# Optimization experiments

Hardware: AMD Instinct MI355X
Metric: run time of the kernel (lower is better)

## Reference

```python
import jax, jax.numpy as jnp
import numpy as np

B, S, HID = 2, 2048, 1024
H, D = 16, 64  # num query heads, head_dim; single shared KV head
SCALE = D ** -0.5


def setup_inputs() -> dict:
    key = jax.random.key(0)
    k1, k2, k3, k4, k5 = jax.random.split(key, 5)
    return {
        "hidden_states": jax.random.normal(k1, (B, S, HID), dtype=jnp.float32),
        "Wq": jax.random.normal(k2, (HID, HID), dtype=jnp.float32) * 0.02,
        "Wk": jax.random.normal(k3, (HID, D), dtype=jnp.float32) * 0.02,
        "Wv": jax.random.normal(k4, (HID, D), dtype=jnp.float32) * 0.02,
        "Wo": jax.random.normal(k5, (HID, HID), dtype=jnp.float32) * 0.02,
    }


def reference(hidden_states, Wq, Wk, Wv, Wo):
    b, s, _ = hidden_states.shape
    # projections: Q has H heads; K/V have a single shared head of dim D
    q = (hidden_states @ Wq).reshape(b, s, H, D)  # [B,S,H,D]
    k = hidden_states @ Wk                        # [B,S,D]
    v = hidden_states @ Wv                        # [B,S,D]
    # scores: broadcast single KV head across all query heads
    scores = jnp.einsum("bqhd,bkd->bhqk", q, k) * SCALE  # [B,H,S,S]
    attn = jax.nn.softmax(scores, axis=-1)
    out = jnp.einsum("bhqk,bkd->bqhd", attn, v).reshape(b, s, HID)
    return out @ Wo
```

## Files before the change

kernel.cpp:

```cpp
#include <hip/hip_runtime.h>
#include <math.h>

#define BATCH 2
#define SEQ   2048
#define HID   1024
#define NH    16
#define HD    64
#define MTOT  (BATCH * SEQ)

#define PST 72
#define WTS 69

#define EXP_C1 0.1803368801111255f
#define EXP_C2 (-17.312340490667562f)

typedef __attribute__((ext_vector_type(8))) short short8;
typedef __attribute__((ext_vector_type(4))) float floatx4;
typedef __attribute__((ext_vector_type(16))) float floatx16;
typedef __attribute__((ext_vector_type(4))) unsigned int uint4v;

#define MFMA32(a, b, c) __builtin_amdgcn_mfma_f32_32x32x16_bf16(a, b, c, 0, 0, 0)

static __device__ __forceinline__ floatx16 zero16() {
    floatx16 z;
    #pragma unroll
    for (int i = 0; i < 16; ++i) z[i] = 0.f;
    return z;
}

__device__ __forceinline__ unsigned short f2bf(float x) {
    unsigned u = __float_as_uint(x);
    u += 0x7FFF + ((u >> 16) & 1);
    return (unsigned short)(u >> 16);
}
__device__ __forceinline__ float bf2f(unsigned short h) {
    return __uint_as_float((unsigned)h << 16);
}
__device__ __forceinline__ unsigned pack2bf(float lo, float hi) {
    return (unsigned)f2bf(lo) | ((unsigned)f2bf(hi) << 16);
}
__device__ __forceinline__ void split16(const float* f, unsigned short* hh, unsigned short* ll) {
    #pragma unroll
    for (int e = 0; e < 16; ++e) {
        unsigned short h = f2bf(f[e]);
        hh[e] = h;
        ll[e] = f2bf(f[e] - bf2f(h));
    }
}

__global__ __launch_bounds__(256)
void presplit_kernel(const float* __restrict__ Wq, const float* __restrict__ Wk,
                     const float* __restrict__ Wv, const float* __restrict__ Wo,
                     const float* __restrict__ X,
                     unsigned short* __restrict__ WqTh, unsigned short* __restrict__ WqTl,
                     unsigned short* __restrict__ WkTh, unsigned short* __restrict__ WkTl,
                     unsigned short* __restrict__ WvTh, unsigned short* __restrict__ WvTl,
                     unsigned short* __restrict__ WoTh, unsigned short* __restrict__ WoTl,
                     unsigned short* __restrict__ Xh)
{
    __shared__ __align__(16) float Wtmp[64][WTS];
    const int tid = threadIdx.x;
    int bx = blockIdx.x;

    if (bx >= 544) {
        size_t i0 = (size_t)(bx - 544) * 4096 + tid * 16;
        float f[16];
        *(float4*)&f[0]  = *(const float4*)(X + i0 + 0);
        *(float4*)&f[4]  = *(const float4*)(X + i0 + 4);
        *(float4*)&f[8]  = *(const float4*)(X + i0 + 8);
        *(float4*)&f[12] = *(const float4*)(X + i0 + 12);
        unsigned short hh[16];
        #pragma unroll
        for (int e = 0; e < 16; ++e) hh[e] = f2bf(f[e]);
        *(uint4*)(Xh + i0)     = *(uint4*)&hh[0];
        *(uint4*)(Xh + i0 + 8) = *(uint4*)&hh[8];
        return;
    }

    const float* W; unsigned short *Th, *Tl; int ldw, kt, nt;
    if (bx < 256)      { W = Wq; Th = WqTh; Tl = WqTl; ldw = HID; kt = bx >> 4; nt = bx & 15; }
    else if (bx < 272) { W = Wk; Th = WkTh; Tl = WkTl; ldw = HD;  kt = bx - 256; nt = 0; }
    else if (bx < 288) { W = Wv; Th = WvTh; Tl = WvTl; ldw = HD;  kt = bx - 272; nt = 0; }
    else               { W = Wo; Th = WoTh; Tl = WoTl; ldw = HID; bx -= 288; kt = bx >> 4; nt = bx & 15; }
    const int k0 = kt * 64, n0 = nt * 64;

    {
        const int wk = tid >> 2, wn = (tid & 3) * 16;
        const float* wp = W + (size_t)(k0 + wk) * ldw + n0 + wn;
        float f[16];
        *(float4*)&f[0]  = *(const float4*)(wp + 0);
        *(float4*)&f[4]  = *(const float4*)(wp + 4);
        *(float4*)&f[8]  = *(const float4*)(wp + 8);
        *(float4*)&f[12] = *(const float4*)(wp + 12);
        #pragma unroll
        for (int e = 0; e < 16; ++e) Wtmp[wk][wn + e] = f[e];
    }
    __syncthreads();
    {
        const int rn = tid >> 2, rk = (tid & 3) * 16;
        float f[16];
        #pragma unroll
        for (int e = 0; e < 16; ++e) f[e] = Wtmp[rk + e][rn];
        unsigned short hh[16], ll[16];
        split16(f, hh, ll);
        size_t off = (size_t)(n0 + rn) * HID + k0 + rk;
        *(uint4*)(Th + off)     = *(uint4*)&hh[0];
        *(uint4*)(Th + off + 8) = *(uint4*)&hh[8];
        *(uint4*)(Tl + off)     = *(uint4*)&ll[0];
        *(uint4*)(Tl + off + 8) = *(uint4*)&ll[8];
    }
}

__global__ __launch_bounds__(256)
void qkv_kernel(const unsigned short* __restrict__ Xh,
                const unsigned short* __restrict__ WqTh, const unsigned short* __restrict__ WqTl,
                const unsigned short* __restrict__ WkTh, const unsigned short* __restrict__ WkTl,
                const unsigned short* __restrict__ WvTh, const unsigned short* __restrict__ WvTl,
                unsigned short* __restrict__ Qh,
                unsigned short* __restrict__ Kh, unsigned short* __restrict__ Vth)
{
    __shared__ __align__(16) unsigned short Ah[128][PST];
    __shared__ __align__(16) unsigned short Wsh[64][PST], Wsl[64][PST];

    const int tid  = threadIdx.x;
    const int wave = tid >> 6, lane = tid & 63;
    const int t = lane & 15, quad = lane >> 4;
    const int m0 = blockIdx.x * 128;
    const int nb = blockIdx.y;

    const unsigned short *WTh, *WTl; int n0b;
    if (nb < 16)       { WTh = WqTh; WTl = WqTl; n0b = nb * 64; }
    else if (nb == 16) { WTh = WkTh; WTl = WkTl; n0b = 0; }
    else               { WTh = WvTh; WTl = WvTl; n0b = 0; }

    floatx4 acc[2][4];
    #pragma unroll
    for (int mi = 0; mi < 2; ++mi)
        #pragma unroll
        for (int sub = 0; sub < 4; ++sub) acc[mi][sub] = (floatx4){0.f,0.f,0.f,0.f};

    for (int kt = 0; kt < HID / 64; ++kt) {
        __syncthreads();
        #pragma unroll
        for (int i = 0; i < 4; ++i) {
            int c = tid + i * 256;
            int row = c >> 3, col8 = (c & 7) * 8;
            *(uint4*)&Ah[row][col8] =
                *(const uint4*)(Xh + (size_t)(m0 + row) * HID + kt * 64 + col8);
        }
        #pragma unroll
        for (int i = 0; i < 2; ++i) {
            int c = tid + i * 256;
            int row = c >> 3, col8 = (c & 7) * 8;
            size_t g = (size_t)(n0b + row) * HID + kt * 64 + col8;
            *(uint4*)&Wsh[row][col8] = *(const uint4*)(WTh + g);
            *(uint4*)&Wsl[row][col8] = *(const uint4*)(WTl + g);
        }
        __syncthreads();
        #pragma unroll
        for (int ks = 0; ks < 2; ++ks) {
            short8 bh[4], bl[4];
            #pragma unroll
            for (int sub = 0; sub < 4; ++sub) {
                bh[sub] = *(const short8*)&Wsh[sub * 16 + t][ks * 32 + quad * 8];
                bl[sub] = *(const short8*)&Wsl[sub * 16 + t][ks * 32 + quad * 8];
            }
            #pragma unroll
            for (int mi = 0; mi < 2; ++mi) {
                short8 ah = *(const short8*)&Ah[wave * 32 + mi * 16 + t][ks * 32 + quad * 8];
                #pragma unroll
                for (int sub = 0; sub < 4; ++sub) {
                    acc[mi][sub] = __builtin_amdgcn_mfma_f32_16x16x32_bf16(ah, bh[sub], acc[mi][sub], 0, 0, 0);
                    acc[mi][sub] = __builtin_amdgcn_mfma_f32_16x16x32_bf16(ah, bl[sub], acc[mi][sub], 0, 0, 0);
                }
            }
        }
    }

    #pragma unroll
    for (int mi = 0; mi < 2; ++mi)
        #pragma unroll
        for (int sub = 0; sub < 4; ++sub)
            #pragma unroll
            for (int r = 0; r < 4; ++r) {
                int g = m0 + wave * 32 + mi * 16 + quad * 4 + r;
                int d = sub * 16 + t;
                unsigned short hh = f2bf(acc[mi][sub][r]);
                if (nb < 16) {
                    int b = g >> 11, s = g & (SEQ - 1);
                    Qh[((size_t)(b * NH + nb) * SEQ + s) * HD + d] = hh;
                } else if (nb == 16) {
                    Kh[(size_t)g * HD + d] = hh;
                } else {
                    int b = g >> 11, s = g & (SEQ - 1);
                    Vth[(size_t)b * HD * SEQ + (size_t)d * SEQ + s] = hh;
                }
            }
}

__global__ __launch_bounds__(256, 2)
void flash_kernel(const unsigned short* __restrict__ Qhg,
                  const unsigned short* __restrict__ Khg,
                  const unsigned short* __restrict__ Vthg,
                  unsigned short* __restrict__ Oh)
{
    __shared__ __align__(16) unsigned short Ksh[64][PST];
    __shared__ __align__(16) unsigned short Vsh[64][PST];

    const int tid  = threadIdx.x;
    const int wave = tid >> 6, lane = tid & 63;
    const int lq = lane & 31, hi = lane >> 5;

    const int q0 = blockIdx.x * 128;
    const int h  = blockIdx.y;
    const int b  = blockIdx.z;

    short8 qreg[4];
    {
        const unsigned short* qp =
            Qhg + ((size_t)(b * NH + h) * SEQ + q0 + wave * 32 + lq) * HD + hi * 8;
        #pragma unroll
        for (int dc = 0; dc < 4; ++dc) qreg[dc] = *(const short8*)(qp + dc * 16);
    }

    const unsigned short* Kh_b  = Khg  + (size_t)b * SEQ * HD;
    const unsigned short* Vth_b = Vthg + (size_t)b * HD * SEQ;

    const int sr = tid >> 3, sc = (tid & 7) * 8;

    float l_part = 0.f;
    floatx16 o0 = zero16(), o1 = zero16();

    uint4 gk0 = *(const uint4*)(Kh_b + (size_t)sr * HD + sc);
    uint4 gk1 = *(const uint4*)(Kh_b + (size_t)(sr + 32) * HD + sc);
    uint4 gv0 = *(const uint4*)(Vth_b + (size_t)sr * SEQ + sc);
    uint4 gv1 = *(const uint4*)(Vth_b + (size_t)(sr + 32) * SEQ + sc);

    for (int kt = 0; kt < SEQ / 64; ++kt) {
        __syncthreads();
        *(uint4*)&Ksh[sr][sc]      = gk0;
        *(uint4*)&Ksh[sr + 32][sc] = gk1;
        *(uint4*)&Vsh[sr][sc]      = gv0;
        *(uint4*)&Vsh[sr + 32][sc] = gv1;
        if (kt + 1 < SEQ / 64) {
            gk0 = *(const uint4*)(Kh_b + (size_t)((kt + 1) * 64 + sr) * HD + sc);
            gk1 = *(const uint4*)(Kh_b + (size_t)((kt + 1) * 64 + sr + 32) * HD + sc);
            gv0 = *(const uint4*)(Vth_b + (size_t)sr * SEQ + (kt + 1) * 64 + sc);
            gv1 = *(const uint4*)(Vth_b + (size_t)(sr + 32) * SEQ + (kt + 1) * 64 + sc);
        }
        __syncthreads();

        floatx16 sf0 = zero16(), sf1 = zero16();
        __builtin_amdgcn_s_setprio(1);
        #pragma unroll
        for (int dc = 0; dc < 4; ++dc) {
            short8 k0 = *(const short8*)&Ksh[lq][dc * 16 + hi * 8];
            short8 k1 = *(const short8*)&Ksh[32 + lq][dc * 16 + hi * 8];
            sf0 = MFMA32(k0, qreg[dc], sf0);
            sf1 = MFMA32(k1, qreg[dc], sf1);
        }
        __builtin_amdgcn_s_setprio(0);

        unsigned w0[8], w1[8];
        #pragma unroll
        for (int kc = 0; kc < 2; ++kc)
            #pragma unroll
            for (int rr = 0; rr < 4; ++rr) {
                float e0 = exp2f(fmaf(kc ? sf1[rr * 4 + 0] : sf0[rr * 4 + 0], EXP_C1, EXP_C2));
                float e1 = exp2f(fmaf(kc ? sf1[rr * 4 + 1] : sf0[rr * 4 + 1], EXP_C1, EXP_C2));
                float e2 = exp2f(fmaf(kc ? sf1[rr * 4 + 2] : sf0[rr * 4 + 2], EXP_C1, EXP_C2));
                float e3 = exp2f(fmaf(kc ? sf1[rr * 4 + 3] : sf0[rr * 4 + 3], EXP_C1, EXP_C2));
                l_part += (e0 + e1) + (e2 + e3);
                w0[kc * 4 + rr] = pack2bf(e0, e1);
                w1[kc * 4 + rr] = pack2bf(e2, e3);
            }

        #pragma unroll
        for (int m = 0; m < 4; ++m) {
            unsigned send0 = hi ? w0[2 * m] : w0[2 * m + 1];
            unsigned send1 = hi ? w1[2 * m] : w1[2 * m + 1];
            unsigned recv0 = (unsigned)__shfl_xor((int)send0, 32);
            unsigned recv1 = (unsigned)__shfl_xor((int)send1, 32);
            unsigned own0 = hi ? w0[2 * m + 1] : w0[2 * m];
            unsigned own1 = hi ? w1[2 * m + 1] : w1[2 * m];
            uint4v pw;
            pw.x = hi ? recv0 : own0;
            pw.y = hi ? recv1 : own1;
            pw.z = hi ? own0 : recv0;
            pw.w = hi ? own1 : recv1;
            short8 pa = __builtin_bit_cast(short8, pw);
            short8 v0 = *(const short8*)&Vsh[lq][m * 16 + hi * 8];
            short8 v1 = *(const short8*)&Vsh[32 + lq][m * 16 + hi * 8];
            __builtin_amdgcn_s_setprio(1);
            o0 = MFMA32(pa, v0, o0);
            o1 = MFMA32(pa, v1, o1);
            __builtin_amdgcn_s_setprio(0);
        }
    }

    float l_full = l_part + __shfl_xor(l_part, 32);
    #pragma unroll
    for (int r = 0; r < 16; ++r) {
        int qr = (r & 3) + 8 * (r >> 2) + 4 * hi;
        float inv = 1.0f / __shfl(l_full, qr);
        size_t row = (size_t)(b * SEQ + q0 + wave * 32 + qr) * HID + h * HD;
        Oh[row + lq]      = f2bf(o0[r] * inv);
        Oh[row + 32 + lq] = f2bf(o1[r] * inv);
    }
}

__global__ __launch_bounds__(256)
void out_proj_kernel(const unsigned short* __restrict__ Ohg,
                     const unsigned short* __restrict__ WoTh,
                     const unsigned short* __restrict__ WoTl,
                     float* __restrict__ out)
{
    __shared__ __align__(16) unsigned short Ah[128][PST];
    __shared__ __align__(16) unsigned short Wsh[64][PST], Wsl[64][PST];

    const int tid  = threadIdx.x;
    const int wave = tid >> 6, lane = tid & 63;
    const int t = lane & 15, quad = lane >> 4;
    const int m0 = blockIdx.x * 128;
    const int n0 = blockIdx.y * 64;

    floatx4 acc[2][4];
    #pragma unroll
    for (int mi = 0; mi < 2; ++mi)
        #pragma unroll
        for (int sub = 0; sub < 4; ++sub) acc[mi][sub] = (floatx4){0.f,0.f,0.f,0.f};

    for (int kt = 0; kt < HID / 64; ++kt) {
        __syncthreads();
        #pragma unroll
        for (int i = 0; i < 4; ++i) {
            int c = tid + i * 256;
            int row = c >> 3, col8 = (c & 7) * 8;
            *(uint4*)&Ah[row][col8] =
                *(const uint4*)(Ohg + (size_t)(m0 + row) * HID + kt * 64 + col8);
        }
        #pragma unroll
        for (int i = 0; i < 2; ++i) {
            int c = tid + i * 256;
            int row = c >> 3, col8 = (c & 7) * 8;
            size_t g = (size_t)(n0 + row) * HID + kt * 64 + col8;
            *(uint4*)&Wsh[row][col8] = *(const uint4*)(WoTh + g);
            *(uint4*)&Wsl[row][col8] = *(const uint4*)(WoTl + g);
        }
        __syncthreads();
        #pragma unroll
        for (int ks = 0; ks < 2; ++ks) {
            short8 bh[4], bl[4];
            #pragma unroll
            for (int sub = 0; sub < 4; ++sub) {
                bh[sub] = *(const short8*)&Wsh[sub * 16 + t][ks * 32 + quad * 8];
                bl[sub] = *(const short8*)&Wsl[sub * 16 + t][ks * 32 + quad * 8];
            }
            #pragma unroll
            for (int mi = 0; mi < 2; ++mi) {
                short8 ah = *(const short8*)&Ah[wave * 32 + mi * 16 + t][ks * 32 + quad * 8];
                #pragma unroll
                for (int sub = 0; sub < 4; ++sub) {
                    acc[mi][sub] = __builtin_amdgcn_mfma_f32_16x16x32_bf16(ah, bh[sub], acc[mi][sub], 0, 0, 0);
                    acc[mi][sub] = __builtin_amdgcn_mfma_f32_16x16x32_bf16(ah, bl[sub], acc[mi][sub], 0, 0, 0);
                }
            }
        }
    }

    #pragma unroll
    for (int mi = 0; mi < 2; ++mi)
        #pragma unroll
        for (int sub = 0; sub < 4; ++sub)
            #pragma unroll
            for (int r = 0; r < 4; ++r)
                out[(size_t)(m0 + wave * 32 + mi * 16 + quad * 4 + r) * HID
                    + n0 + sub * 16 + t] = acc[mi][sub][r];
}

extern "C" void kernel_launch(void* const* d_in, const int* in_sizes, int n_in,
                              void* d_out, int out_size, void* d_ws, size_t ws_size,
                              hipStream_t stream)
{
    const float* X  = (const float*)d_in[0];
    const float* Wq = (const float*)d_in[1];
    const float* Wk = (const float*)d_in[2];
    const float* Wv = (const float*)d_in[3];
    const float* Wo = (const float*)d_in[4];
    float* out = (float*)d_out;

    unsigned short* Qh = (unsigned short*)d_out;
    unsigned short* Xh = Qh + (size_t)BATCH * NH * SEQ * HD;

    char* ws = (char*)d_ws;
    const size_t SZ_WQ = (size_t)HID * HID * 2;
    const size_t SZ_WK = (size_t)HD * HID * 2;
    unsigned short* WqTh = (unsigned short*)(ws);
    unsigned short* WqTl = (unsigned short*)(ws + SZ_WQ);
    unsigned short* WkTh = (unsigned short*)(ws + 2*SZ_WQ);
    unsigned short* WkTl = (unsigned short*)(ws + 2*SZ_WQ + SZ_WK);
    unsigned short* WvTh = (unsigned short*)(ws + 2*SZ_WQ + 2*SZ_WK);
    unsigned short* WvTl = (unsigned short*)(ws + 2*SZ_WQ + 3*SZ_WK);
    unsigned short* WoTh = (unsigned short*)(ws + 2*SZ_WQ + 4*SZ_WK);
    unsigned short* WoTl = (unsigned short*)(ws + 3*SZ_WQ + 4*SZ_WK);
    unsigned short* Kh   = (unsigned short*)(ws + 4*SZ_WQ + 4*SZ_WK);
    unsigned short* Vth  = (unsigned short*)(ws + 4*SZ_WQ + 4*SZ_WK + (size_t)MTOT*HD*2);
    unsigned short* Oh   = (unsigned short*)(ws + 4*SZ_WQ + 4*SZ_WK + (size_t)MTOT*HD*4);

    presplit_kernel<<<dim3(1568), 256, 0, stream>>>(Wq, Wk, Wv, Wo, X,
        WqTh, WqTl, WkTh, WkTl, WvTh, WvTl, WoTh, WoTl, Xh);
    qkv_kernel<<<dim3(MTOT / 128, 18), 256, 0, stream>>>(Xh,
        WqTh, WqTl, WkTh, WkTl, WvTh, WvTl, Qh, Kh, Vth);
    flash_kernel<<<dim3(SEQ / 128, NH, BATCH), 256, 0, stream>>>(Qh, Kh, Vth, Oh);
    out_proj_kernel<<<dim3(MTOT / 128, HID / 64), 256, 0, stream>>>(Oh, WoTh, WoTl, out);
}
```

Baseline: 206.1 us.

## Split flash-attention KV tile across wave pairs and truncate softmax weights

The flash kernel now launches 512 threads. Each pair of waves shares a 32-row query slice, and each wave of the pair handles half of every 64-key tile. Their partial outputs and row sums are reduced through shared memory at the end. The softmax weights are also packed to bf16 by truncation (bit masking) rather than round-to-nearest, and the row sum uses the truncated values so it stays consistent. The change aims to raise per-block parallelism and cut the per-wave work and register pressure, at the cost of an extra shared-memory reduction and slightly less accurate weight rounding.

```diff
diff --git a/kernel.cpp b/kernel.cpp
--- a/kernel.cpp
+++ b/kernel.cpp
@@ -35,9 +35,6 @@
 }
 __device__ __forceinline__ float bf2f(unsigned short h) {
     return __uint_as_float((unsigned)h << 16);
-}
-__device__ __forceinline__ unsigned pack2bf(float lo, float hi) {
-    return (unsigned)f2bf(lo) | ((unsigned)f2bf(hi) << 16);
 }
 __device__ __forceinline__ void split16(const float* f, unsigned short* hh, unsigned short* ll) {
     #pragma unroll
@@ -198,18 +195,21 @@
             }
 }
 
-__global__ __launch_bounds__(256, 2)
+__global__ __launch_bounds__(512, 4)
 void flash_kernel(const unsigned short* __restrict__ Qhg,
                   const unsigned short* __restrict__ Khg,
                   const unsigned short* __restrict__ Vthg,
                   unsigned short* __restrict__ Oh)
 {
-    __shared__ __align__(16) unsigned short Ksh[64][PST];
-    __shared__ __align__(16) unsigned short Vsh[64][PST];
+    __shared__ __align__(16) char smem[33792];
+    unsigned short (*Ksh)[PST] = (unsigned short (*)[PST])smem;
+    unsigned short (*Vsh)[PST] = (unsigned short (*)[PST])(smem + 64 * PST * 2);
 
     const int tid  = threadIdx.x;
     const int wave = tid >> 6, lane = tid & 63;
     const int lq = lane & 31, hi = lane >> 5;
+    const int qw = wave >> 1;
+    const int ks = wave & 1;
 
     const int q0 = blockIdx.x * 128;
     const int h  = blockIdx.y;
@@ -218,7 +218,7 @@
     short8 qreg[4];
     {
         const unsigned short* qp =
-            Qhg + ((size_t)(b * NH + h) * SEQ + q0 + wave * 32 + lq) * HD + hi * 8;
+            Qhg + ((size_t)(b * NH + h) * SEQ + q0 + qw * 32 + lq) * HD + hi * 8;
         #pragma unroll
         for (int dc = 0; dc < 4; ++dc) qreg[dc] = *(const short8*)(qp + dc * 16);
     }
@@ -231,66 +231,57 @@
     float l_part = 0.f;
     floatx16 o0 = zero16(), o1 = zero16();
 
-    uint4 gk0 = *(const uint4*)(Kh_b + (size_t)sr * HD + sc);
-    uint4 gk1 = *(const uint4*)(Kh_b + (size_t)(sr + 32) * HD + sc);
-    uint4 gv0 = *(const uint4*)(Vth_b + (size_t)sr * SEQ + sc);
-    uint4 gv1 = *(const uint4*)(Vth_b + (size_t)(sr + 32) * SEQ + sc);
+    uint4 gk = *(const uint4*)(Kh_b + (size_t)sr * HD + sc);
+    uint4 gv = *(const uint4*)(Vth_b + (size_t)sr * SEQ + sc);
 
     for (int kt = 0; kt < SEQ / 64; ++kt) {
         __syncthreads();
-        *(uint4*)&Ksh[sr][sc]      = gk0;
-        *(uint4*)&Ksh[sr + 32][sc] = gk1;
-        *(uint4*)&Vsh[sr][sc]      = gv0;
-        *(uint4*)&Vsh[sr + 32][sc] = gv1;
+        *(uint4*)&Ksh[sr][sc] = gk;
+        *(uint4*)&Vsh[sr][sc] = gv;
         if (kt + 1 < SEQ / 64) {
-            gk0 = *(const uint4*)(Kh_b + (size_t)((kt + 1) * 64 + sr) * HD + sc);
-            gk1 = *(const uint4*)(Kh_b + (size_t)((kt + 1) * 64 + sr + 32) * HD + sc);
-            gv0 = *(const uint4*)(Vth_b + (size_t)sr * SEQ + (kt + 1) * 64 + sc);
-            gv1 = *(const uint4*)(Vth_b + (size_t)(sr + 32) * SEQ + (kt + 1) * 64 + sc);
-        }
-        __syncthreads();
-
-        floatx16 sf0 = zero16(), sf1 = zero16();
+            gk = *(const uint4*)(Kh_b + (size_t)((kt + 1) * 64 + sr) * HD + sc);
+            gv = *(const uint4*)(Vth_b + (size_t)sr * SEQ + (kt + 1) * 64 + sc);
+        }
+        __syncthreads();
+
+        floatx16 sf = zero16();
         __builtin_amdgcn_s_setprio(1);
         #pragma unroll
         for (int dc = 0; dc < 4; ++dc) {
-            short8 k0 = *(const short8*)&Ksh[lq][dc * 16 + hi * 8];
-            short8 k1 = *(const short8*)&Ksh[32 + lq][dc * 16 + hi * 8];
-            sf0 = MFMA32(k0, qreg[dc], sf0);
-            sf1 = MFMA32(k1, qreg[dc], sf1);
+            short8 kf = *(const short8*)&Ksh[ks * 32 + lq][dc * 16 + hi * 8];
+            sf = MFMA32(kf, qreg[dc], sf);
         }
         __builtin_amdgcn_s_setprio(0);
 
-        unsigned w0[8], w1[8];
-        #pragma unroll
-        for (int kc = 0; kc < 2; ++kc)
-            #pragma unroll
-            for (int rr = 0; rr < 4; ++rr) {
-                float e0 = exp2f(fmaf(kc ? sf1[rr * 4 + 0] : sf0[rr * 4 + 0], EXP_C1, EXP_C2));
-                float e1 = exp2f(fmaf(kc ? sf1[rr * 4 + 1] : sf0[rr * 4 + 1], EXP_C1, EXP_C2));
-                float e2 = exp2f(fmaf(kc ? sf1[rr * 4 + 2] : sf0[rr * 4 + 2], EXP_C1, EXP_C2));
-                float e3 = exp2f(fmaf(kc ? sf1[rr * 4 + 3] : sf0[rr * 4 + 3], EXP_C1, EXP_C2));
-                l_part += (e0 + e1) + (e2 + e3);
-                w0[kc * 4 + rr] = pack2bf(e0, e1);
-                w1[kc * 4 + rr] = pack2bf(e2, e3);
-            }
-
-        #pragma unroll
-        for (int m = 0; m < 4; ++m) {
-            unsigned send0 = hi ? w0[2 * m] : w0[2 * m + 1];
-            unsigned send1 = hi ? w1[2 * m] : w1[2 * m + 1];
+        unsigned w0[4], w1[4];
+        #pragma unroll
+        for (int rr = 0; rr < 4; ++rr) {
+            unsigned u0 = __float_as_uint(exp2f(fmaf(sf[rr * 4 + 0], EXP_C1, EXP_C2)));
+            unsigned u1 = __float_as_uint(exp2f(fmaf(sf[rr * 4 + 1], EXP_C1, EXP_C2)));
+            unsigned u2 = __float_as_uint(exp2f(fmaf(sf[rr * 4 + 2], EXP_C1, EXP_C2)));
+            unsigned u3 = __float_as_uint(exp2f(fmaf(sf[rr * 4 + 3], EXP_C1, EXP_C2)));
+            l_part += __uint_as_float(u0 & 0xFFFF0000u) + __uint_as_float(u1 & 0xFFFF0000u)
+                    + __uint_as_float(u2 & 0xFFFF0000u) + __uint_as_float(u3 & 0xFFFF0000u);
+            w0[rr] = (u0 >> 16) | (u1 & 0xFFFF0000u);
+            w1[rr] = (u2 >> 16) | (u3 & 0xFFFF0000u);
+        }
+
+        #pragma unroll
+        for (int mm = 0; mm < 2; ++mm) {
+            unsigned send0 = hi ? w0[2 * mm] : w0[2 * mm + 1];
+            unsigned send1 = hi ? w1[2 * mm] : w1[2 * mm + 1];
             unsigned recv0 = (unsigned)__shfl_xor((int)send0, 32);
             unsigned recv1 = (unsigned)__shfl_xor((int)send1, 32);
-            unsigned own0 = hi ? w0[2 * m + 1] : w0[2 * m];
-            unsigned own1 = hi ? w1[2 * m + 1] : w1[2 * m];
+            unsigned own0 = hi ? w0[2 * mm + 1] : w0[2 * mm];
+            unsigned own1 = hi ? w1[2 * mm + 1] : w1[2 * mm];
             uint4v pw;
             pw.x = hi ? recv0 : own0;
             pw.y = hi ? recv1 : own1;
             pw.z = hi ? own0 : recv0;
             pw.w = hi ? own1 : recv1;
             short8 pa = __builtin_bit_cast(short8, pw);
-            short8 v0 = *(const short8*)&Vsh[lq][m * 16 + hi * 8];
-            short8 v1 = *(const short8*)&Vsh[32 + lq][m * 16 + hi * 8];
+            short8 v0 = *(const short8*)&Vsh[lq][ks * 32 + mm * 16 + hi * 8];
+            short8 v1 = *(const short8*)&Vsh[32 + lq][ks * 32 + mm * 16 + hi * 8];
             __builtin_amdgcn_s_setprio(1);
             o0 = MFMA32(pa, v0, o0);
             o1 = MFMA32(pa, v1, o1);
@@ -298,14 +289,28 @@
         }
     }
 
-    float l_full = l_part + __shfl_xor(l_part, 32);
-    #pragma unroll
-    for (int r = 0; r < 16; ++r) {
-        int qr = (r & 3) + 8 * (r >> 2) + 4 * hi;
-        float inv = 1.0f / __shfl(l_full, qr);
-        size_t row = (size_t)(b * SEQ + q0 + wave * 32 + qr) * HID + h * HD;
-        Oh[row + lq]      = f2bf(o0[r] * inv);
-        Oh[row + 32 + lq] = f2bf(o1[r] * inv);
+    float l_wave = l_part + __shfl_xor(l_part, 32);
+    __syncthreads();
+    float* cb = (float*)smem;
+    const int cbase = (qw * 64 + lane) * 33;
+    if (ks) {
+        #pragma unroll
+        for (int r = 0; r < 16; ++r) { cb[cbase + r] = o0[r]; cb[cbase + 16 + r] = o1[r]; }
+        cb[cbase + 32] = l_wave;
+    }
+    __syncthreads();
+    if (!ks) {
+        float l_tot = l_wave + cb[cbase + 32];
+        #pragma unroll
+        for (int r = 0; r < 16; ++r) {
+            int qr = (r & 3) + 8 * (r >> 2) + 4 * hi;
+            float inv = 1.0f / __shfl(l_tot, qr);
+            float a0 = o0[r] + cb[cbase + r];
+            float a1 = o1[r] + cb[cbase + 16 + r];
+            size_t row = (size_t)(b * SEQ + q0 + qw * 32 + qr) * HID + h * HD;
+            Oh[row + lq]      = f2bf(a0 * inv);
+            Oh[row + 32 + lq] = f2bf(a1 * inv);
+        }
     }
 }
 
@@ -411,6 +416,6 @@
         WqTh, WqTl, WkTh, WkTl, WvTh, WvTl, WoTh, WoTl, Xh);
     qkv_kernel<<<dim3(MTOT / 128, 18), 256, 0, stream>>>(Xh,
         WqTh, WqTl, WkTh, WkTl, WvTh, WvTl, Qh, Kh, Vth);
-    flash_kernel<<<dim3(SEQ / 128, NH, BATCH), 256, 0, stream>>>(Qh, Kh, Vth, Oh);
+    flash_kernel<<<dim3(SEQ / 128, NH, BATCH), 512, 0, stream>>>(Qh, Kh, Vth, Oh);
     out_proj_kernel<<<dim3(MTOT / 128, HID / 64), 256, 0, stream>>>(Oh, WoTh, WoTl, out);
 }
```

Measured after the change: 199.4 us. 3.2% less time.
